# Kernel optimization log

Hardware: AMD Instinct MI355X
Metric: run time of the kernel (lower is better)

Reference implementation:

```python
import jax, jax.numpy as jnp
import numpy as np

N, E, IN, H, C, T = 50000, 800000, 128, 64, 64, 2
F1, FO1 = H, H // T   # conv1: per-tower in/out feats
F2, FO2 = H, C // T   # conv2
STD_EPS = 1e-5
BN_EPS = 1e-5


def setup_inputs() -> dict:
    key = jax.random.key(0)
    ks = jax.random.split(key, 12)
    rn = lambda k, s, sc=0.05: jax.random.normal(k, s, jnp.float32) * sc
    return {
        "x": jax.random.normal(ks[0], (N, IN), jnp.float32),
        "embed_W": rn(ks[1], (IN, H)),
        "embed_b": jnp.zeros((H,), jnp.float32),
        "pre_W1": rn(ks[2], (T, 2 * F1, F1)),
        "pre_b1": jnp.zeros((T, F1), jnp.float32),
        "post_W1": rn(ks[3], (T, 13 * F1, FO1)),
        "post_b1": jnp.zeros((T, FO1), jnp.float32),
        "lin_W1": rn(ks[4], (H, H)),
        "lin_b1": jnp.zeros((H,), jnp.float32),
        "bn_gamma": jnp.ones((H,), jnp.float32),
        "bn_beta": jnp.zeros((H,), jnp.float32),
        "pre_W2": rn(ks[5], (T, 2 * F2, F2)),
        "pre_b2": jnp.zeros((T, F2), jnp.float32),
        "post_W2": rn(ks[6], (T, 13 * F2, FO2)),
        "post_b2": jnp.zeros((T, FO2), jnp.float32),
        "lin_W2": rn(ks[7], (C, C)),
        "lin_b2": jnp.zeros((C,), jnp.float32),
        "src": jax.random.randint(ks[8], (E,), 0, N, jnp.int32),
        "dst": jax.random.randint(ks[9], (E,), 0, N, jnp.int32),
    }


def _pna_conv(h, src, dst, deg_raw, degc, avg_log, preW, preb, postW, postb, linW, linb):
    # h: [N, F] node feats; messages flow src -> dst, aggregated at dst.
    m = jnp.concatenate([h[dst], h[src]], axis=-1)            # [E, 2F]  (cat[x_i, x_j])
    m = jnp.einsum('ef,tfg->etg', m, preW) + preb[None]       # [E, T, F] per-tower pre-NN
    seg = lambda v: jax.ops.segment_sum(v, dst, num_segments=N)
    cnt = degc[:, None, None]                                 # clamped degree >= 1
    has = (deg_raw > 0)[:, None, None]
    mean = seg(m) / cnt                                       # [N, T, F]
    mean_sq = seg(m * m) / cnt
    mn = jnp.where(has, jax.ops.segment_min(m, dst, num_segments=N), 0.0)
    mx = jnp.where(has, jax.ops.segment_max(m, dst, num_segments=N), 0.0)
    std = jnp.sqrt(jax.nn.relu(mean_sq - mean * mean) + STD_EPS)
    agg = jnp.concatenate([mean, mn, mx, std], axis=-1)       # [N, T, 4F]
    ld = jnp.log(degc + 1.0)[:, None, None]
    out = jnp.concatenate([agg, agg * (ld / avg_log), agg * (avg_log / ld)], axis=-1)  # [N, T, 12F]
    F = h.shape[-1]
    out = jnp.concatenate([jnp.broadcast_to(h[:, None, :], (N, T, F)), out], axis=-1)  # [N, T, 13F]
    out = jnp.einsum('ntf,tfg->ntg', out, postW) + postb[None]  # [N, T, FO] per-tower post-NN
    return out.reshape(N, -1) @ linW + linb                    # final mixing Linear(out, out)


def reference(x, embed_W, embed_b, pre_W1, pre_b1, post_W1, post_b1, lin_W1, lin_b1,
              bn_gamma, bn_beta, pre_W2, pre_b2, post_W2, post_b2, lin_W2, lin_b2,
              src, dst):
    deg_raw = jax.ops.segment_sum(jnp.ones((E,), jnp.float32), dst, num_segments=N)
    degc = jnp.maximum(deg_raw, 1.0)
    avg_log = jnp.mean(jnp.log(deg_raw + 1.0))  # avg_deg['log'] from the graph's degrees
    h = x @ embed_W + embed_b
    h = _pna_conv(h, src, dst, deg_raw, degc, avg_log,
                  pre_W1, pre_b1, post_W1, post_b1, lin_W1, lin_b1)
    mu = jnp.mean(h, axis=0)
    var = jnp.mean((h - mu) ** 2, axis=0)
    h = bn_gamma * (h - mu) / jnp.sqrt(var + BN_EPS) + bn_beta
    h = jax.nn.relu(h)  # dropout is identity in eval mode
    return _pna_conv(h, src, dst, deg_raw, degc, avg_log,
                     pre_W2, pre_b2, post_W2, post_b2, lin_W2, lin_b2)
```

## Files before the change

### kernel.cpp

```cpp
#include <hip/hip_runtime.h>
#include <hip/hip_fp16.h>

#define N_NODES 50000
#define E_EDGES 800000
#define IN_F    128
#define H_F     64
#define STD_EPS 1e-5f
#define BN_EPS  1e-5f

#define HIST_BLK 3125
#define EMB_BLK  768
#define SCAN_BLK 49
#define TRANS_BLK 448

typedef __attribute__((ext_vector_type(8))) short bf16x8;
typedef __attribute__((ext_vector_type(4))) float f32x4;

__device__ __forceinline__ unsigned bf16_rne(float f) {
  unsigned u = __float_as_uint(f);
  return (u + 0x7fffu + ((u >> 16) & 1u)) >> 16;
}
__device__ __forceinline__ void bf16_split2(float x, float y, unsigned& hi, unsigned& lo) {
  unsigned hx = bf16_rne(x), hy = bf16_rne(y);
  float rx = x - __uint_as_float(hx << 16);
  float ry = y - __uint_as_float(hy << 16);
  hi = hx | (hy << 16);
  lo = bf16_rne(rx) | (bf16_rne(ry) << 16);
}

#define MFMA(acc, a, b) acc = __builtin_amdgcn_mfma_f32_16x16x32_bf16(a, b, acc, 0, 0, 0)

__global__ __launch_bounds__(256) void k_hist_embed(const int* __restrict__ dst,
                                                    int* __restrict__ deg,
                                                    const float* __restrict__ x,
                                                    const float* __restrict__ W,
                                                    const float* __restrict__ bias,
                                                    float* __restrict__ h) {
  __shared__ float sW[IN_F * 64];
  __shared__ float sx[IN_F * 36];
  if (blockIdx.x < HIST_BLK) {
    int e = blockIdx.x * 256 + threadIdx.x;
    atomicAdd(&deg[dst[e]], 1);
    return;
  }
  for (int i = threadIdx.x; i < IN_F * 64; i += 256) sW[i] = W[i];
  int f = threadIdx.x & 63, ng = threadIdx.x >> 6;
  float bj = bias[f];
  const int NGRP = (N_NODES + 31) / 32;
  for (int grp = blockIdx.x - HIST_BLK; grp < NGRP; grp += EMB_BLK) {
    int n0 = grp * 32;
    __syncthreads();
    for (int idx = threadIdx.x; idx < 32 * IN_F; idx += 256) {
      int nl = idx >> 7, k = idx & 127;
      int n = n0 + nl;
      sx[k * 36 + nl] = (n < N_NODES) ? x[(size_t)n * IN_F + k] : 0.f;
    }
    __syncthreads();
    float a[8] = {bj, bj, bj, bj, bj, bj, bj, bj};
    const float* xp = &sx[ng * 8];
#pragma unroll 4
    for (int k = 0; k < IN_F; k++) {
      float4 h0 = *(const float4*)&xp[k * 36];
      float4 h1 = *(const float4*)&xp[k * 36 + 4];
      float w = sW[k * 64 + f];
      a[0] = fmaf(h0.x, w, a[0]); a[1] = fmaf(h0.y, w, a[1]);
      a[2] = fmaf(h0.z, w, a[2]); a[3] = fmaf(h0.w, w, a[3]);
      a[4] = fmaf(h1.x, w, a[4]); a[5] = fmaf(h1.y, w, a[5]);
      a[6] = fmaf(h1.z, w, a[6]); a[7] = fmaf(h1.w, w, a[7]);
    }
#pragma unroll
    for (int j = 0; j < 8; j++) {
      int n = n0 + ng * 8 + j;
      if (n < N_NODES) h[(size_t)n * 64 + f] = a[j];
    }
  }
}

__global__ __launch_bounds__(256) void k_scanpart_trans(const int* __restrict__ deg,
                                                        int* __restrict__ partials,
                                                        float* __restrict__ scalars,
                                                        const float* __restrict__ pW1,
                                                        const float* __restrict__ pW2,
                                                        const float* __restrict__ lW1,
                                                        const float* __restrict__ lW2,
                                                        unsigned short* __restrict__ WBhi,
                                                        unsigned short* __restrict__ WBlo,
                                                        float* __restrict__ lWT) {
  __shared__ int red[256];
  __shared__ float redf[256];
  if (blockIdx.x < SCAN_BLK) {
    int base = blockIdx.x * 1024;
    int s = 0; float ls = 0.f;
    for (int j = threadIdx.x; j < 1024; j += 256) {
      int i = base + j;
      if (i < N_NODES) { int d = deg[i]; s += d; ls += logf((float)d + 1.0f); }
    }
    red[threadIdx.x] = s; redf[threadIdx.x] = ls; __syncthreads();
    for (int st = 128; st > 0; st >>= 1) {
      if (threadIdx.x < st) {
        red[threadIdx.x] += red[threadIdx.x + st];
        redf[threadIdx.x] += redf[threadIdx.x + st];
      }
      __syncthreads();
    }
    if (threadIdx.x == 0) {
      partials[blockIdx.x] = red[0];
      atomicAdd(&scalars[0], redf[0]);
    }
    return;
  }
  int idx = (blockIdx.x - SCAN_BLK) * 256 + threadIdx.x;
  if (idx < 106496) {
    int f = idx % 832;
    int rest = idx / 832;
    int col = rest & 31, tt = rest >> 5;
    const float* srcp = (tt >= 2) ? pW2 : pW1;
    float v = srcp[((size_t)(tt & 1) * 832 + f) * 32 + col];
    unsigned hb = bf16_rne(v);
    float rsd = v - __uint_as_float(hb << 16);
    WBhi[idx] = (unsigned short)hb;
    WBlo[idx] = (unsigned short)bf16_rne(rsd);
  } else if (idx < 114688) {
    int jj = idx - 106496;
    int layer = jj / 4096, r2 = jj % 4096;
    int c4 = r2 / 256, r3 = r2 % 256;
    int col = r3 / 4, j = r3 % 4;
    const float* srcl = layer ? lW2 : lW1;
    lWT[jj] = srcl[(c4 * 4 + j) * 64 + col];
  }
}

__global__ __launch_bounds__(256) void k_scan_final(const int* __restrict__ deg,
                                                    const int* __restrict__ partials,
                                                    int* __restrict__ row_ptr,
                                                    int* __restrict__ cursor,
                                                    float* __restrict__ scalars) {
  __shared__ int ts[256];
  __shared__ int sbase;
  if (threadIdx.x == 0) {
    int pre = 0;
    for (int b = 0; b < (int)blockIdx.x; b++) pre += partials[b];
    sbase = pre;
    if (blockIdx.x == 0) {
      scalars[1] = scalars[0] / (float)N_NODES;
      row_ptr[N_NODES] = E_EDGES;
    }
  }
  int base = blockIdx.x * 1024 + threadIdx.x * 4;
  int d[4]; int s = 0;
#pragma unroll
  for (int j = 0; j < 4; j++) {
    int i = base + j;
    d[j] = (i < N_NODES) ? deg[i] : 0;
    s += d[j];
  }
  ts[threadIdx.x] = s; __syncthreads();
  for (int off = 1; off < 256; off <<= 1) {
    int t = (threadIdx.x >= off) ? ts[threadIdx.x - off] : 0;
    __syncthreads();
    ts[threadIdx.x] += t;
    __syncthreads();
  }
  int excl = (threadIdx.x > 0) ? ts[threadIdx.x - 1] : 0;
  int run = sbase + excl;
#pragma unroll
  for (int j = 0; j < 4; j++) {
    int i = base + j;
    if (i < N_NODES) { row_ptr[i] = run; cursor[i] = run; run += d[j]; }
  }
}

__global__ __launch_bounds__(256) void k_scatter(const int* __restrict__ src,
                                                 const int* __restrict__ dst,
                                                 int* __restrict__ cursor,
                                                 int* __restrict__ csr_src) {
  int e = blockIdx.x * 256 + threadIdx.x;
  if (e < E_EDGES) {
    int d = dst[e];
    int p = atomicAdd(&cursor[d], 1);
    csr_src[p] = src[e];
  }
}

template <bool BN>
__global__ __launch_bounds__(256) void k_preab(const float* __restrict__ hin,
                                               const float* __restrict__ preW,
                                               const float* __restrict__ preb,
                                               const float* __restrict__ bnsum,
                                               const float* __restrict__ bnsumsq,
                                               const float* __restrict__ gamma,
                                               const float* __restrict__ beta,
                                               float* __restrict__ h2out,
                                               float* __restrict__ hA,
                                               __half* __restrict__ hB) {
  __shared__ float sWp[64 * 128];
  __shared__ float sh[64 * 68];
  __shared__ float sbn[128];
  int t = blockIdx.x & 1;
  const float* Wsrc = preW + (size_t)t * 128 * 64;
  for (int i = threadIdx.x; i < 64 * 64; i += 256) {
    int k = i >> 6, f = i & 63;
    float wa = Wsrc[k * 64 + f];
    float wb = Wsrc[(64 + k) * 64 + f];
    *(float2*)&sWp[k * 128 + f * 2] = make_float2(wa, wb);
  }
  if (BN && threadIdx.x < 64) {
    int c = threadIdx.x;
    float mu = bnsum[c] * (1.f / N_NODES);
    float var = bnsumsq[c] * (1.f / N_NODES) - mu * mu;
    float sc = gamma[c] / sqrtf(var + BN_EPS);
    sbn[c] = sc;
    sbn[64 + c] = fmaf(-mu, sc, beta[c]);
  }
  int f = threadIdx.x & 63, ng = threadIdx.x >> 6;
  float pb = preb[t * 64 + f];
  int nblk2 = gridDim.x >> 1;
  const int NGRP = (N_NODES + 63) / 64;
  for (int grp = blockIdx.x >> 1; grp < NGRP; grp += nblk2) {
    int n0 = grp * 64;
    __syncthreads();
    for (int idx = threadIdx.x; idx < 64 * 64; idx += 256) {
      int nl = idx >> 6, k = idx & 63;
      int n = n0 + nl;
      float v = 0.f;
      if (n < N_NODES) {
        v = hin[(size_t)n * 64 + k];
        if (BN) {
          v = fmaxf(fmaf(v, sbn[k], sbn[64 + k]), 0.f);
          if (t == 0) h2out[(size_t)n * 64 + k] = v;
        }
      }
      sh[k * 68 + nl] = v;
    }
    __syncthreads();
    float a[16], b[16];
#pragma unroll
    for (int j = 0; j < 16; j++) { a[j] = pb; b[j] = 0.f; }
    const float* hp = &sh[ng * 16];
    const float* wp = &sWp[f * 2];
#pragma unroll 2
    for (int k = 0; k < 64; k++) {
      float4 h0 = *(const float4*)&hp[k * 68];
      float4 h1 = *(const float4*)&hp[k * 68 + 4];
      float4 h2 = *(const float4*)&hp[k * 68 + 8];
      float4 h3 = *(const float4*)&hp[k * 68 + 12];
      float2 w2 = *(const float2*)&wp[k * 128];
      a[0]  = fmaf(h0.x, w2.x, a[0]);  b[0]  = fmaf(h0.x, w2.y, b[0]);
      a[1]  = fmaf(h0.y, w2.x, a[1]);  b[1]  = fmaf(h0.y, w2.y, b[1]);
      a[2]  = fmaf(h0.z, w2.x, a[2]);  b[2]  = fmaf(h0.z, w2.y, b[2]);
      a[3]  = fmaf(h0.w, w2.x, a[3]);  b[3]  = fmaf(h0.w, w2.y, b[3]);
      a[4]  = fmaf(h1.x, w2.x, a[4]);  b[4]  = fmaf(h1.x, w2.y, b[4]);
      a[5]  = fmaf(h1.y, w2.x, a[5]);  b[5]  = fmaf(h1.y, w2.y, b[5]);
      a[6]  = fmaf(h1.z, w2.x, a[6]);  b[6]  = fmaf(h1.z, w2.y, b[6]);
      a[7]  = fmaf(h1.w, w2.x, a[7]);  b[7]  = fmaf(h1.w, w2.y, b[7]);
      a[8]  = fmaf(h2.x, w2.x, a[8]);  b[8]  = fmaf(h2.x, w2.y, b[8]);
      a[9]  = fmaf(h2.y, w2.x, a[9]);  b[9]  = fmaf(h2.y, w2.y, b[9]);
      a[10] = fmaf(h2.z, w2.x, a[10]); b[10] = fmaf(h2.z, w2.y, b[10]);
      a[11] = fmaf(h2.w, w2.x, a[11]); b[11] = fmaf(h2.w, w2.y, b[11]);
      a[12] = fmaf(h3.x, w2.x, a[12]); b[12] = fmaf(h3.x, w2.y, b[12]);
      a[13] = fmaf(h3.y, w2.x, a[13]); b[13] = fmaf(h3.y, w2.y, b[13]);
      a[14] = fmaf(h3.z, w2.x, a[14]); b[14] = fmaf(h3.z, w2.y, b[14]);
      a[15] = fmaf(h3.w, w2.x, a[15]); b[15] = fmaf(h3.w, w2.y, b[15]);
    }
    int tf = t * 64 + f;
#pragma unroll
    for (int j = 0; j < 16; j++) {
      int n = n0 + ng * 16 + j;
      if (n < N_NODES) {
        hA[(size_t)n * 128 + tf] = a[j];
        hB[(size_t)n * 128 + tf] = __float2half(b[j]);
      }
    }
  }
}

#define GATHER8(D0,D1,D2,D3,D4,D5,D6,D7, bb, rl)                              \
  { int _s0 = __builtin_amdgcn_readfirstlane(csr_src[min((bb)+0,(rl))]);      \
    int _s1 = __builtin_amdgcn_readfirstlane(csr_src[min((bb)+1,(rl))]);      \
    int _s2 = __builtin_amdgcn_readfirstlane(csr_src[min((bb)+2,(rl))]);      \
    int _s3 = __builtin_amdgcn_readfirstlane(csr_src[min((bb)+3,(rl))]);      \
    int _s4 = __builtin_amdgcn_readfirstlane(csr_src[min((bb)+4,(rl))]);      \
    int _s5 = __builtin_amdgcn_readfirstlane(csr_src[min((bb)+5,(rl))]);      \
    int _s6 = __builtin_amdgcn_readfirstlane(csr_src[min((bb)+6,(rl))]);      \
    int _s7 = __builtin_amdgcn_readfirstlane(csr_src[min((bb)+7,(rl))]);      \
    D0 = hB2[((size_t)_s0 << 6) + oh2];                                       \
    D1 = hB2[((size_t)_s1 << 6) + oh2];                                       \
    D2 = hB2[((size_t)_s2 << 6) + oh2];                                       \
    D3 = hB2[((size_t)_s3 << 6) + oh2];                                       \
    D4 = hB2[((size_t)_s4 << 6) + oh2];                                       \
    D5 = hB2[((size_t)_s5 << 6) + oh2];                                       \
    D6 = hB2[((size_t)_s6 << 6) + oh2];                                       \
    D7 = hB2[((size_t)_s7 << 6) + oh2]; }

#define EDGE1(vv, P, S)                                                       \
  { float2 _f = __half22float2(vv);                                           \
    P##sx##S += _f.x; P##qx##S = fmaf(_f.x, _f.x, P##qx##S);                  \
    P##mnx##S = fminf(P##mnx##S, _f.x); P##mxx##S = fmaxf(P##mxx##S, _f.x);   \
    P##sy##S += _f.y; P##qy##S = fmaf(_f.y, _f.y, P##qy##S);                  \
    P##mny##S = fminf(P##mny##S, _f.y); P##mxy##S = fmaxf(P##mxy##S, _f.y); }

#define COMP8(A0,A1,A2,A3,A4,A5,A6,A7, m8, dg, P)                             \
  { if ((m8)+0 < (dg)) EDGE1(A0, P, 0);                                       \
    if ((m8)+1 < (dg)) EDGE1(A1, P, 1);                                       \
    if ((m8)+2 < (dg)) EDGE1(A2, P, 0);                                       \
    if ((m8)+3 < (dg)) EDGE1(A3, P, 1);                                       \
    if ((m8)+4 < (dg)) EDGE1(A4, P, 0);                                       \
    if ((m8)+5 < (dg)) EDGE1(A5, P, 1);                                       \
    if ((m8)+6 < (dg)) EDGE1(A6, P, 0);                                       \
    if ((m8)+7 < (dg)) EDGE1(A7, P, 1); }

#define FINALIZE(P, dg, a, hs, nl)                                            \
  { float cnt = (float)((dg) > 0 ? (dg) : 1);                                 \
    float inv = 1.0f / cnt;                                                   \
    float mrx = (P##sx0 + P##sx1) * inv, mry = (P##sy0 + P##sy1) * inv;       \
    float sdx = sqrtf(fmaxf((P##qx0 + P##qx1) * inv - mrx * mrx, 0.f) + STD_EPS); \
    float sdy = sqrtf(fmaxf((P##qy0 + P##qy1) * inv - mry * mry, 0.f) + STD_EPS); \
    float mnx = fminf(P##mnx0, P##mnx1), mny = fminf(P##mny0, P##mny1);       \
    float mxx = fmaxf(P##mxx0, P##mxx1), mxy = fmaxf(P##mxy0, P##mxy1);       \
    float ax = (a).x, ay = (a).y;                                             \
    if ((dg) == 0) { mnx = 0; mny = 0; mxx = 0; mxy = 0; ax = 0; ay = 0; }    \
    float meanx = mrx + ax, meany = mry + ay;                                 \
    mnx += ax; mny += ay; mxx += ax; mxy += ay;                               \
    unsigned* ahp = &sAhi[(t * 8 + (nl)) * 160];                              \
    unsigned* alp = &sAlo[(t * 8 + (nl)) * 160];                              \
    int sw = ((nl) & 7) << 2;                                                 \
    int p = lane & 31;                                                        \
    unsigned hi, lo;                                                          \
    bf16_split2((hs).x, (hs).y, hi, lo); ahp[p ^ sw] = hi; alp[p ^ sw] = lo;  \
    bf16_split2(meanx, meany, hi, lo); ahp[(p+32) ^ sw] = hi; alp[(p+32) ^ sw] = lo; \
    bf16_split2(mnx, mny, hi, lo);     ahp[(p+64) ^ sw] = hi; alp[(p+64) ^ sw] = lo; \
    bf16_split2(mxx, mxy, hi, lo);     ahp[(p+96) ^ sw] = hi; alp[(p+96) ^ sw] = lo; \
    bf16_split2(sdx, sdy, hi, lo);     ahp[(p+128) ^ sw] = hi; alp[(p+128) ^ sw] = lo; }

__global__ __launch_bounds__(256, 6) void k_conv(const float* __restrict__ hA,
                                                 const __half* __restrict__ hB,
                                                 const float* __restrict__ hskip,
                                                 const int* __restrict__ row_ptr,
                                                 const int* __restrict__ csr_src,
                                                 const unsigned short* __restrict__ WBhi,
                                                 const unsigned short* __restrict__ WBlo,
                                                 const float* __restrict__ postb,
                                                 const float* __restrict__ linWT,
                                                 const float* __restrict__ linb,
                                                 const float* __restrict__ scalars,
                                                 float* __restrict__ out) {
  __shared__ unsigned sAhi[2560];
  __shared__ unsigned sAlo[2560];
  int w = threadIdx.x >> 6, lane = threadIdx.x & 63;
  int n0 = blockIdx.x * 8;
  int t = lane >> 5, fb2 = (lane & 31) * 2;
  int off = t * 64 + fb2;
  float avg = scalars[1];

  const __half2* hB2 = (const __half2*)hB;
  int oh2 = (t << 5) | (lane & 31);

  int nu = n0 + w * 2;
  float2 au = *(const float2*)&hA[(size_t)nu * 128 + off];
  float2 av = *(const float2*)&hA[(size_t)(nu + 1) * 128 + off];
  float2 hsu = *(const float2*)&hskip[(size_t)nu * 64 + fb2];
  float2 hsv = *(const float2*)&hskip[(size_t)(nu + 1) * 64 + fb2];
  int rpu0 = __builtin_amdgcn_readfirstlane(row_ptr[nu]);
  int rpu1 = __builtin_amdgcn_readfirstlane(row_ptr[nu + 1]);
  int rpv1 = __builtin_amdgcn_readfirstlane(row_ptr[nu + 2]);
  int dgu = rpu1 - rpu0, dgv = rpv1 - rpu1;
  int rlu = rpu1 - 1, rlv = rpv1 - 1;
  int nbu = (dgu + 7) >> 3, nbv = (dgv + 7) >> 3;
  int M = nbu > nbv ? nbu : nbv;

  float usx0=0,uqx0=0,usy0=0,uqy0=0, usx1=0,uqx1=0,usy1=0,uqy1=0;
  float umnx0=INFINITY,umny0=INFINITY,umxx0=-INFINITY,umxy0=-INFINITY;
  float umnx1=INFINITY,umny1=INFINITY,umxx1=-INFINITY,umxy1=-INFINITY;
  float vsx0=0,vqx0=0,vsy0=0,vqy0=0, vsx1=0,vqx1=0,vsy1=0,vqy1=0;
  float vmnx0=INFINITY,vmny0=INFINITY,vmxx0=-INFINITY,vmxy0=-INFINITY;
  float vmnx1=INFINITY,vmny1=INFINITY,vmxx1=-INFINITY,vmxy1=-INFINITY;

  __half2 UA0{},UA1{},UA2{},UA3{},UA4{},UA5{},UA6{},UA7{};
  __half2 UB0{},UB1{},UB2{},UB3{},UB4{},UB5{},UB6{},UB7{};
  __half2 VA0{},VA1{},VA2{},VA3{},VA4{},VA5{},VA6{},VA7{};
  __half2 VB0{},VB1{},VB2{},VB3{},VB4{},VB5{},VB6{},VB7{};

  if (nbu > 0) GATHER8(UA0,UA1,UA2,UA3,UA4,UA5,UA6,UA7, rpu0, rlu);
  if (nbv > 0) GATHER8(VA0,VA1,VA2,VA3,VA4,VA5,VA6,VA7, rpu1, rlv);
#pragma unroll 1
  for (int m = 0; m < M; m++) {
    int bu = rpu0 + m * 8 + 8, bv = rpu1 + m * 8 + 8;
    if (m + 1 < nbu) GATHER8(UB0,UB1,UB2,UB3,UB4,UB5,UB6,UB7, bu, rlu);
    if (m + 1 < nbv) GATHER8(VB0,VB1,VB2,VB3,VB4,VB5,VB6,VB7, bv, rlv);
    int m8 = m << 3;
    if (m < nbu) COMP8(UA0,UA1,UA2,UA3,UA4,UA5,UA6,UA7, m8, dgu, u);
    if (m < nbv) COMP8(VA0,VA1,VA2,VA3,VA4,VA5,VA6,VA7, m8, dgv, v);
    UA0=UB0;UA1=UB1;UA2=UB2;UA3=UB3;UA4=UB4;UA5=UB5;UA6=UB6;UA7=UB7;
    VA0=VB0;VA1=VB1;VA2=VB2;VA3=VB3;VA4=VB4;VA5=VB5;VA6=VB6;VA7=VB7;
  }

  FINALIZE(u, dgu, au, hsu, w * 2);
  FINALIZE(v, dgv, av, hsv, w * 2 + 1);
  __syncthreads();

  f32x4 acc1 = {0.f, 0.f, 0.f, 0.f};
  f32x4 acc2 = {0.f, 0.f, 0.f, 0.f};
  f32x4 acc3 = {0.f, 0.f, 0.f, 0.f};
  int tw = w >> 1, ntile = w & 1;
  int kq = lane >> 4;
  int rsw = lane & 7;
  {
    const bf16x8* Ah = (const bf16x8*)(sAhi + (tw * 8 + (lane & 7)) * 160);
    const bf16x8* Al = (const bf16x8*)(sAlo + (tw * 8 + (lane & 7)) * 160);
    int brow = (tw * 32 + ntile * 16 + (lane & 15)) * 104 + kq;
    const bf16x8* Bh = (const bf16x8*)WBhi + brow;
    const bf16x8* Bl = (const bf16x8*)WBlo + brow;
    bf16x8 bh_0 = Bh[0], bl_0 = Bl[0];
    bf16x8 bh_1 = Bh[4], bl_1 = Bl[4];
#pragma unroll
    for (int s = 0; s < 10; s++) {
      bf16x8 bh_n, bl_n;
      if (s < 8) { bh_n = Bh[(s + 2) * 4]; bl_n = Bl[(s + 2) * 4]; }
      bf16x8 ah = Ah[(s * 4 + kq) ^ rsw], al = Al[(s * 4 + kq) ^ rsw];
      MFMA(acc1, ah, bh_0); MFMA(acc1, al, bh_0); MFMA(acc1, ah, bl_0);
      bh_0 = bh_1; bl_0 = bl_1; bh_1 = bh_n; bl_1 = bl_n;
    }
    bf16x8 c_0 = Bh[40], d_0 = Bh[72];
    bf16x8 c_1 = Bh[44], d_1 = Bh[76];
#pragma unroll
    for (int s = 0; s < 8; s++) {
      bf16x8 c_n, d_n;
      if (s < 6) { c_n = Bh[48 + s * 4]; d_n = Bh[80 + s * 4]; }
      bf16x8 ah = Ah[((s + 2) * 4 + kq) ^ rsw], al = Al[((s + 2) * 4 + kq) ^ rsw];
      MFMA(acc2, ah, c_0); MFMA(acc2, al, c_0);
      MFMA(acc3, ah, d_0); MFMA(acc3, al, d_0);
      c_0 = c_1; d_0 = d_1; c_1 = c_n; d_1 = d_n;
    }
  }
  __syncthreads();

  float* spo = (float*)sAhi;
  if (lane < 32) {
    int colg = tw * 32 + ntile * 16 + (lane & 15);
    float pbv = postb[colg];
    int rbase = kq * 4;
    int rb = n0 + rbase;
    int p0 = row_ptr[rb], p1 = row_ptr[rb+1], p2 = row_ptr[rb+2],
        p3 = row_ptr[rb+3], p4 = row_ptr[rb+4];
    int dgv4[4] = {p1 - p0, p2 - p1, p3 - p2, p4 - p3};
#pragma unroll
    for (int r = 0; r < 4; r++) {
      float cnt = (float)(dgv4[r] > 0 ? dgv4[r] : 1);
      float ldv = logf(cnt + 1.f);
      spo[(rbase + r) * 64 + colg] =
          acc1[r] + (ldv / avg) * acc2[r] + (avg / ldv) * acc3[r] + pbv;
    }
  }
  __syncthreads();

  {
    float la0 = linb[lane], la1 = la0;
    const float4* lw4 = (const float4*)linWT + lane;
    const float* p0 = &spo[(w * 2) * 64];
    const float* p1 = p0 + 64;
#pragma unroll
    for (int c4 = 0; c4 < 16; c4++) {
      float4 lwv = lw4[c4 * 64];
      float4 pa = *(const float4*)&p0[c4 * 4];
      float4 pb2 = *(const float4*)&p1[c4 * 4];
      la0 = fmaf(pa.w, lwv.w, fmaf(pa.z, lwv.z, fmaf(pa.y, lwv.y, fmaf(pa.x, lwv.x, la0))));
      la1 = fmaf(pb2.w, lwv.w, fmaf(pb2.z, lwv.z, fmaf(pb2.y, lwv.y, fmaf(pb2.x, lwv.x, la1))));
    }
    size_t ob = (size_t)(n0 + w * 2) * 64 + lane;
    out[ob] = la0;
    out[ob + 64] = la1;
  }
}

__global__ __launch_bounds__(256) void k_bnstats(const float* __restrict__ y,
                                                 float* __restrict__ bnsum,
                                                 float* __restrict__ bnsumsq) {
  __shared__ float r1[256], r2[256];
  int c = threadIdx.x & 63, r = threadIdx.x >> 6;
  float s = 0, q = 0;
  for (int n = blockIdx.x * 4 + r; n < N_NODES; n += gridDim.x * 4) {
    float v = y[(size_t)n * 64 + c];
    s += v; q = fmaf(v, v, q);
  }
  r1[threadIdx.x] = s; r2[threadIdx.x] = q; __syncthreads();
  if (threadIdx.x < 64) {
    s = r1[threadIdx.x] + r1[threadIdx.x + 64] + r1[threadIdx.x + 128] + r1[threadIdx.x + 192];
    q = r2[threadIdx.x] + r2[threadIdx.x + 64] + r2[threadIdx.x + 128] + r2[threadIdx.x + 192];
    atomicAdd(&bnsum[threadIdx.x], s);
    atomicAdd(&bnsumsq[threadIdx.x], q);
  }
}

extern "C" void kernel_launch(void* const* d_in, const int* in_sizes, int n_in,
                              void* d_out, int out_size, void* d_ws, size_t ws_size,
                              hipStream_t stream) {
  const float* x      = (const float*)d_in[0];
  const float* embW   = (const float*)d_in[1];
  const float* embB   = (const float*)d_in[2];
  const float* preW1  = (const float*)d_in[3];
  const float* preb1  = (const float*)d_in[4];
  const float* postW1 = (const float*)d_in[5];
  const float* postb1 = (const float*)d_in[6];
  const float* linW1  = (const float*)d_in[7];
  const float* linb1  = (const float*)d_in[8];
  const float* gamma  = (const float*)d_in[9];
  const float* beta   = (const float*)d_in[10];
  const float* preW2  = (const float*)d_in[11];
  const float* preb2  = (const float*)d_in[12];
  const float* postW2 = (const float*)d_in[13];
  const float* postb2 = (const float*)d_in[14];
  const float* linW2  = (const float*)d_in[15];
  const float* linb2  = (const float*)d_in[16];
  const int*   src    = (const int*)d_in[17];
  const int*   dst    = (const int*)d_in[18];
  float* out = (float*)d_out;

  char* w = (char*)d_ws;
  size_t o = 0;
  int*   deg     = (int*)(w + o);   o += (size_t)N_NODES * 4;
  float* scalars = (float*)(w + o); o += 64;
  float* bnsum   = (float*)(w + o); o += 256;
  float* bnsumsq = (float*)(w + o); o += 256;
  size_t zero_len = o;
  o = (o + 255) & ~(size_t)255;
  int* partials = (int*)(w + o);  o += 256;
  int* row_ptr  = (int*)(w + o);  o += (size_t)(N_NODES + 1) * 4; o = (o + 255) & ~(size_t)255;
  int* cursor   = (int*)(w + o);  o += (size_t)N_NODES * 4;       o = (o + 255) & ~(size_t)255;
  int* csr      = (int*)(w + o);  o += (size_t)E_EDGES * 4;       o = (o + 255) & ~(size_t)255;
  unsigned short* WBhi = (unsigned short*)(w + o); o += (size_t)2 * 53248 * 2;
  unsigned short* WBlo = (unsigned short*)(w + o); o += (size_t)2 * 53248 * 2;
  float* linWT  = (float*)(w + o); o += (size_t)2 * 4096 * 4;
  float* h1 = (float*)(w + o); o += (size_t)N_NODES * 64 * 4;
  float* y1 = (float*)(w + o); o += (size_t)N_NODES * 64 * 4;
  float* h2 = (float*)(w + o); o += (size_t)N_NODES * 64 * 4;
  float* hA = (float*)(w + o); o += (size_t)N_NODES * 128 * 4;
  __half* hBh = (__half*)(w + o); o += (size_t)N_NODES * 128 * 2;

  hipMemsetAsync(w, 0, zero_len, stream);

  k_hist_embed<<<HIST_BLK + EMB_BLK, 256, 0, stream>>>(dst, deg, x, embW, embB, h1);
  k_scanpart_trans<<<SCAN_BLK + TRANS_BLK, 256, 0, stream>>>(
      deg, partials, scalars, postW1, postW2, linW1, linW2, WBhi, WBlo, linWT);
  k_scan_final<<<SCAN_BLK, 256, 0, stream>>>(deg, partials, row_ptr, cursor, scalars);
  k_scatter<<<(E_EDGES + 255) / 256, 256, 0, stream>>>(src, dst, cursor, csr);

  k_preab<false><<<768, 256, 0, stream>>>(h1, preW1, preb1, nullptr, nullptr,
                                          nullptr, nullptr, nullptr, hA, hBh);
  k_conv<<<N_NODES / 8, 256, 0, stream>>>(hA, hBh, h1, row_ptr, csr,
                                          WBhi, WBlo, postb1, linWT, linb1, scalars, y1);
  k_bnstats<<<256, 256, 0, stream>>>(y1, bnsum, bnsumsq);
  k_preab<true><<<768, 256, 0, stream>>>(y1, preW2, preb2, bnsum, bnsumsq,
                                         gamma, beta, h2, hA, hBh);
  k_conv<<<N_NODES / 8, 256, 0, stream>>>(hA, hBh, h2, row_ptr, csr,
                                          WBhi + 53248, WBlo + 53248, postb2,
                                          linWT + 4096, linb2, scalars, out);
}
```

Baseline: 570.4 us.

## Split fused conv kernel into separate aggregation and post-MLP kernels

The fused k_conv kernel, which gathered neighbour features, reduced them and ran the MFMA post-NN, is split into k_agg (128-thread blocks, writing mean/min/max/std to a global [N,512] fp32 buffer) and k_post (reloads the aggregates and skip features into LDS as split bf16 and runs the GEMM). The aim is to let the latency-bound gather run at higher occupancy without the GEMM's LDS and register footprint. In exchange it adds roughly 100 MB of extra global write plus read traffic per conv and two more kernel launches.

New measurement: 717.6 us. 25.8% more time.

```diff
diff --git a/kernel.cpp b/kernel.cpp
--- a/kernel.cpp
+++ b/kernel.cpp
@@ -283,14 +283,14 @@
     int _s5 = __builtin_amdgcn_readfirstlane(csr_src[min((bb)+5,(rl))]);      \
     int _s6 = __builtin_amdgcn_readfirstlane(csr_src[min((bb)+6,(rl))]);      \
     int _s7 = __builtin_amdgcn_readfirstlane(csr_src[min((bb)+7,(rl))]);      \
-    D0 = hB2[((size_t)_s0 << 6) + oh2];                                       \
-    D1 = hB2[((size_t)_s1 << 6) + oh2];                                       \
-    D2 = hB2[((size_t)_s2 << 6) + oh2];                                       \
-    D3 = hB2[((size_t)_s3 << 6) + oh2];                                       \
-    D4 = hB2[((size_t)_s4 << 6) + oh2];                                       \
-    D5 = hB2[((size_t)_s5 << 6) + oh2];                                       \
-    D6 = hB2[((size_t)_s6 << 6) + oh2];                                       \
-    D7 = hB2[((size_t)_s7 << 6) + oh2]; }
+    D0 = hB2[((size_t)_s0 << 6) + lane];                                      \
+    D1 = hB2[((size_t)_s1 << 6) + lane];                                      \
+    D2 = hB2[((size_t)_s2 << 6) + lane];                                      \
+    D3 = hB2[((size_t)_s3 << 6) + lane];                                      \
+    D4 = hB2[((size_t)_s4 << 6) + lane];                                      \
+    D5 = hB2[((size_t)_s5 << 6) + lane];                                      \
+    D6 = hB2[((size_t)_s6 << 6) + lane];                                      \
+    D7 = hB2[((size_t)_s7 << 6) + lane]; }
 
 #define EDGE1(vv, P, S)                                                       \
   { float2 _f = __half22float2(vv);                                           \
@@ -309,7 +309,7 @@
     if ((m8)+6 < (dg)) EDGE1(A6, P, 0);                                       \
     if ((m8)+7 < (dg)) EDGE1(A7, P, 1); }
 
-#define FINALIZE(P, dg, a, hs, nl)                                            \
+#define FINALIZE_G(P, dg, a, n)                                               \
   { float cnt = (float)((dg) > 0 ? (dg) : 1);                                 \
     float inv = 1.0f / cnt;                                                   \
     float mrx = (P##sx0 + P##sx1) * inv, mry = (P##sy0 + P##sy1) * inv;       \
@@ -319,47 +319,25 @@
     float mxx = fmaxf(P##mxx0, P##mxx1), mxy = fmaxf(P##mxy0, P##mxy1);       \
     float ax = (a).x, ay = (a).y;                                             \
     if ((dg) == 0) { mnx = 0; mny = 0; mxx = 0; mxy = 0; ax = 0; ay = 0; }    \
-    float meanx = mrx + ax, meany = mry + ay;                                 \
-    mnx += ax; mny += ay; mxx += ax; mxy += ay;                               \
-    unsigned* ahp = &sAhi[(t * 8 + (nl)) * 160];                              \
-    unsigned* alp = &sAlo[(t * 8 + (nl)) * 160];                              \
-    int sw = ((nl) & 7) << 2;                                                 \
-    int p = lane & 31;                                                        \
-    unsigned hi, lo;                                                          \
-    bf16_split2((hs).x, (hs).y, hi, lo); ahp[p ^ sw] = hi; alp[p ^ sw] = lo;  \
-    bf16_split2(meanx, meany, hi, lo); ahp[(p+32) ^ sw] = hi; alp[(p+32) ^ sw] = lo; \
-    bf16_split2(mnx, mny, hi, lo);     ahp[(p+64) ^ sw] = hi; alp[(p+64) ^ sw] = lo; \
-    bf16_split2(mxx, mxy, hi, lo);     ahp[(p+96) ^ sw] = hi; alp[(p+96) ^ sw] = lo; \
-    bf16_split2(sdx, sdy, hi, lo);     ahp[(p+128) ^ sw] = hi; alp[(p+128) ^ sw] = lo; }
-
-__global__ __launch_bounds__(256, 6) void k_conv(const float* __restrict__ hA,
-                                                 const __half* __restrict__ hB,
-                                                 const float* __restrict__ hskip,
-                                                 const int* __restrict__ row_ptr,
-                                                 const int* __restrict__ csr_src,
-                                                 const unsigned short* __restrict__ WBhi,
-                                                 const unsigned short* __restrict__ WBlo,
-                                                 const float* __restrict__ postb,
-                                                 const float* __restrict__ linWT,
-                                                 const float* __restrict__ linb,
-                                                 const float* __restrict__ scalars,
-                                                 float* __restrict__ out) {
-  __shared__ unsigned sAhi[2560];
-  __shared__ unsigned sAlo[2560];
+    float* ap = &agg[(size_t)(n) * 512 + off];                                \
+    *(float2*)&ap[0]   = make_float2(mrx + ax, mry + ay);                     \
+    *(float2*)&ap[128] = make_float2(mnx + ax, mny + ay);                     \
+    *(float2*)&ap[256] = make_float2(mxx + ax, mxy + ay);                     \
+    *(float2*)&ap[384] = make_float2(sdx, sdy); }
+
+__global__ __launch_bounds__(128, 8) void k_agg(const float* __restrict__ hA,
+                                                const __half* __restrict__ hB,
+                                                const int* __restrict__ row_ptr,
+                                                const int* __restrict__ csr_src,
+                                                float* __restrict__ agg) {
   int w = threadIdx.x >> 6, lane = threadIdx.x & 63;
-  int n0 = blockIdx.x * 8;
   int t = lane >> 5, fb2 = (lane & 31) * 2;
   int off = t * 64 + fb2;
-  float avg = scalars[1];
-
   const __half2* hB2 = (const __half2*)hB;
-  int oh2 = (t << 5) | (lane & 31);
-
-  int nu = n0 + w * 2;
+
+  int nu = (blockIdx.x * 2 + w) * 2;
   float2 au = *(const float2*)&hA[(size_t)nu * 128 + off];
   float2 av = *(const float2*)&hA[(size_t)(nu + 1) * 128 + off];
-  float2 hsu = *(const float2*)&hskip[(size_t)nu * 64 + fb2];
-  float2 hsv = *(const float2*)&hskip[(size_t)(nu + 1) * 64 + fb2];
   int rpu0 = __builtin_amdgcn_readfirstlane(row_ptr[nu]);
   int rpu1 = __builtin_amdgcn_readfirstlane(row_ptr[nu + 1]);
   int rpv1 = __builtin_amdgcn_readfirstlane(row_ptr[nu + 2]);
@@ -394,8 +372,49 @@
     VA0=VB0;VA1=VB1;VA2=VB2;VA3=VB3;VA4=VB4;VA5=VB5;VA6=VB6;VA7=VB7;
   }
 
-  FINALIZE(u, dgu, au, hsu, w * 2);
-  FINALIZE(v, dgv, av, hsv, w * 2 + 1);
+  FINALIZE_G(u, dgu, au, nu);
+  FINALIZE_G(v, dgv, av, nu + 1);
+}
+
+__global__ __launch_bounds__(256, 6) void k_post(const float* __restrict__ agg,
+                                                 const float* __restrict__ hskip,
+                                                 const int* __restrict__ row_ptr,
+                                                 const unsigned short* __restrict__ WBhi,
+                                                 const unsigned short* __restrict__ WBlo,
+                                                 const float* __restrict__ postb,
+                                                 const float* __restrict__ linWT,
+                                                 const float* __restrict__ linb,
+                                                 const float* __restrict__ scalars,
+                                                 float* __restrict__ out) {
+  __shared__ unsigned sAhi[2560];
+  __shared__ unsigned sAlo[2560];
+  int w = threadIdx.x >> 6, lane = threadIdx.x & 63;
+  int n0 = blockIdx.x * 8;
+  float avg = scalars[1];
+
+#pragma unroll
+  for (int r = 0; r < 2; r++) {
+    int idx = r * 256 + (int)threadIdx.x;
+    int nl = idx >> 6, p2 = idx & 63;
+    int tt = p2 >> 5, col = p2 & 31;
+    float2 v = *(const float2*)&hskip[(size_t)(n0 + nl) * 64 + col * 2];
+    unsigned hi, lo;
+    bf16_split2(v.x, v.y, hi, lo);
+    int d = (tt * 8 + nl) * 160 + (col ^ ((nl & 7) << 2));
+    sAhi[d] = hi; sAlo[d] = lo;
+  }
+#pragma unroll
+  for (int r = 0; r < 8; r++) {
+    int idx = r * 256 + (int)threadIdx.x;
+    int nl = idx >> 8, rr = idx & 255;
+    int s = rr >> 6, p2 = rr & 63;
+    int tt = p2 >> 5, col = p2 & 31;
+    float2 v = *(const float2*)&agg[(size_t)(n0 + nl) * 512 + s * 128 + p2 * 2];
+    unsigned hi, lo;
+    bf16_split2(v.x, v.y, hi, lo);
+    int d = (tt * 8 + nl) * 160 + ((((s + 1) * 32) + col) ^ ((nl & 7) << 2));
+    sAhi[d] = hi; sAlo[d] = lo;
+  }
   __syncthreads();
 
   f32x4 acc1 = {0.f, 0.f, 0.f, 0.f};
@@ -535,6 +554,7 @@
   float* h2 = (float*)(w + o); o += (size_t)N_NODES * 64 * 4;
   float* hA = (float*)(w + o); o += (size_t)N_NODES * 128 * 4;
   __half* hBh = (__half*)(w + o); o += (size_t)N_NODES * 128 * 2;
+  float* agg = (float*)(w + o); o += (size_t)N_NODES * 512 * 4;
 
   hipMemsetAsync(w, 0, zero_len, stream);
 
@@ -546,12 +566,14 @@
 
   k_preab<false><<<768, 256, 0, stream>>>(h1, preW1, preb1, nullptr, nullptr,
                                           nullptr, nullptr, nullptr, hA, hBh);
-  k_conv<<<N_NODES / 8, 256, 0, stream>>>(hA, hBh, h1, row_ptr, csr,
+  k_agg<<<N_NODES / 4, 128, 0, stream>>>(hA, hBh, row_ptr, csr, agg);
+  k_post<<<N_NODES / 8, 256, 0, stream>>>(agg, h1, row_ptr,
                                           WBhi, WBlo, postb1, linWT, linb1, scalars, y1);
   k_bnstats<<<256, 256, 0, stream>>>(y1, bnsum, bnsumsq);
   k_preab<true><<<768, 256, 0, stream>>>(y1, preW2, preb2, bnsum, bnsumsq,
                                          gamma, beta, h2, hA, hBh);
-  k_conv<<<N_NODES / 8, 256, 0, stream>>>(hA, hBh, h2, row_ptr, csr,
+  k_agg<<<N_NODES / 4, 128, 0, stream>>>(hA, hBh, row_ptr, csr, agg);
+  k_post<<<N_NODES / 8, 256, 0, stream>>>(agg, h2, row_ptr,
                                           WBhi + 53248, WBlo + 53248, postb2,
                                           linWT + 4096, linb2, scalars, out);
 }
```
